# Kernel tuning notes

Hardware: AMD Instinct MI355X
Metric: run time of the kernel (lower is better)

## Reference

```python
import jax, jax.numpy as jnp
import numpy as np

B, S, D, d, O = 64, 196, 64, 2, 10  # batch, sites, bond_dim, feature dim, labels


def setup_inputs() -> dict:
    key = jax.random.key(0)
    k1, k2, k3 = jax.random.split(key, 3)
    x = jax.random.uniform(k1, (B, S, d), dtype=jnp.float32)
    # 'random_eye' init: identity on the bond indices (broadcast over input
    # index) plus small noise, so the untrained chain is well-conditioned.
    eye_cores = jnp.broadcast_to(jnp.eye(D, dtype=jnp.float32)[None, :, :, None], (S, D, D, d))
    cores = eye_cores + 0.01 * jax.random.normal(k2, (S, D, D, d), dtype=jnp.float32)
    out_core = 0.1 * jax.random.normal(k3, (O, D, D), dtype=jnp.float32)
    return {"x": x, "cores": cores, "out_core": out_core}


def _chain_matmul(mats):
    """Log-depth product of a chain of batched matrices. mats: [b, s, D, D]."""
    b, s, Dm, _ = mats.shape
    p = 1
    while p < s:
        p *= 2
    if p != s:  # pad with identities up to a power of two
        pad = jnp.broadcast_to(jnp.eye(Dm, dtype=mats.dtype), (b, p - s, Dm, Dm))
        mats = jnp.concatenate([mats, pad], axis=1)
    while mats.shape[1] > 1:  # pairwise tree reduction (log2(s) steps)
        mats = jnp.matmul(mats[:, 0::2], mats[:, 1::2])
    return mats[:, 0]  # [b, D, D]


def reference(x, cores, out_core):
    # InputRegion.forward: contract each site's feature vector with its core
    mats = jnp.einsum('slri,bsi->bslr', cores, x)  # [b, s, D, D]
    half = mats.shape[1] // 2  # output core sits at the chain center
    left = _chain_matmul(mats[:, :half])    # [b, D, D]
    right = _chain_matmul(mats[:, half:])   # [b, D, D]
    # Open boundary conditions: boundary vectors e0 = [1, 0, ..., 0]
    lvec = left[:, 0, :]   # e0 @ left  -> [b, D]
    rvec = right[:, :, 0]  # right @ e0 -> [b, D]
    # Contract through the central output core to get class scores
    return jnp.einsum('bl,olr,br->bo', lvec, out_core, rvec)  # [b, O]
```

## Files before the change

kernel.cpp:

```cpp
#include <hip/hip_runtime.h>

namespace {
constexpr int NB = 64, NS = 196, ND = 64, NO = 10;
constexpr int EPAIRS = NS * ND * ND;
constexpr size_t EBYTES = (size_t)EPAIRS * 4;


#define BARRIER() asm volatile("s_waitcnt lgkmcnt(0)\n\ts_barrier" ::: "memory")

#define U0(w_) __builtin_bit_cast(float, (unsigned)((w_) << 16))
#define U1(w_) __builtin_bit_cast(float, (unsigned)((w_) & 0xFFFF0000u))

__device__ __forceinline__ unsigned bf16rne(float f) {
    const unsigned b = __builtin_bit_cast(unsigned, f);
    return (b + 0x7FFFu + ((b >> 16) & 1u)) >> 16;
}

__global__ __launch_bounds__(256) void mps_conv_kernel(
    const float* __restrict__ cores, unsigned* __restrict__ etab)
{
    const int p = blockIdx.x * 256 + threadIdx.x;
    const int rem = p & 4095;
    const int l = rem >> 6, r = rem & 63;
    const float2 c = ((const float2*)cores)[p];
    const float sub = (l == r) ? 1.0f : 0.0f;
    etab[p] = bf16rne(c.x - sub) | (bf16rne(c.y - sub) << 16);
}

#define LLOAD(BUF, SITE) do {                                                 \
  const unsigned* _p = gL + (size_t)(SITE) * 4096;                            \
  _Pragma("unroll") for (int i = 0; i < 16; ++i)                              \
    BUF[i] = *(const uint2*)(_p + i * 64);                                    \
} while (0)

#define LSTEP(P, BUF, S) do {                                                 \
  const float2 xc = *(const float2*)(xlds + 2 * (S));                         \
  const float s0 = xc.x + xc.y;                                               \
  float4 vv[4];                                                               \
  _Pragma("unroll") for (int m = 0; m < 4; ++m)                               \
    vv[m] = ((const float4*)(vbuf[P] + 16 * q))[m];                           \
  const float2 yo = *(const float2*)(vbuf[P] + c0);                           \
  float a00a = 0.f, a10a = 0.f, a01a = 0.f, a11a = 0.f;                       \
  float a00b = 0.f, a10b = 0.f, a01b = 0.f, a11b = 0.f;                       \
  _Pragma("unroll") for (int i = 0; i < 16; i += 2) {                         \
    { const float vl = vv[i >> 2][i & 3]; const uint2 W = BUF[i];             \
      a00a = fmaf(vl, U0(W.x), a00a); a10a = fmaf(vl, U1(W.x), a10a);         \
      a01a = fmaf(vl, U0(W.y), a01a); a11a = fmaf(vl, U1(W.y), a11a); }       \
    { const float vl = vv[(i + 1) >> 2][(i + 1) & 3]; const uint2 W = BUF[i + 1]; \
      a00b = fmaf(vl, U0(W.x), a00b); a10b = fmaf(vl, U1(W.x), a10b);         \
      a01b = fmaf(vl, U0(W.y), a01b); a11b = fmaf(vl, U1(W.y), a11b); }       \
  }                                                                           \
  float a00 = a00a + a00b, a10 = a10a + a10b;                                 \
  float a01 = a01a + a01b, a11 = a11a + a11b;                                 \
  a00 += __shfl_xor(a00, 16, 64); a00 += __shfl_xor(a00, 32, 64);             \
  a10 += __shfl_xor(a10, 16, 64); a10 += __shfl_xor(a10, 32, 64);             \
  a01 += __shfl_xor(a01, 16, 64); a01 += __shfl_xor(a01, 32, 64);             \
  a11 += __shfl_xor(a11, 16, 64); a11 += __shfl_xor(a11, 32, 64);             \
  if (q == 0) {                                                               \
    float2 yn;                                                                \
    yn.x = fmaf(s0, yo.x, fmaf(xc.x, a00, xc.y * a10));                       \
    yn.y = fmaf(s0, yo.y, fmaf(xc.x, a01, xc.y * a11));                       \
    *(float2*)(vbuf[(P) ^ 1] + c0) = yn;                                      \
  }                                                                           \
} while (0)

#define RLOAD(BUF, SITE) do {                                                 \
  const unsigned* _p = gR + (size_t)(SITE) * 4096;                            \
  _Pragma("unroll") for (int m = 0; m < 8; ++m)                               \
    BUF[m] = *(const uint4*)(_p + m * 4);                                     \
} while (0)

#define RSTEP(P, BUF, K) do {                                                 \
  const float2 xc = *(const float2*)(xlds + 2 * (195 - (K)));                 \
  const float s0 = xc.x + xc.y;                                               \
  float4 vv[8];                                                               \
  _Pragma("unroll") for (int m = 0; m < 8; ++m)                               \
    vv[m] = ((const float4*)(vbuf[P] + 32 * h))[m];                           \
  const float yo = vbuf[P][row];                                              \
  float a0a = 0.f, a1a = 0.f, a0b = 0.f, a1b = 0.f;                           \
  _Pragma("unroll") for (int m = 0; m < 8; m += 2) {                          \
    { const uint4 W = BUF[m]; const float4 V = vv[m];                         \
      a0a = fmaf(V.x, U0(W.x), a0a); a1a = fmaf(V.x, U1(W.x), a1a);           \
      a0a = fmaf(V.y, U0(W.y), a0a); a1a = fmaf(V.y, U1(W.y), a1a);           \
      a0a = fmaf(V.z, U0(W.z), a0a); a1a = fmaf(V.z, U1(W.z), a1a);           \
      a0a = fmaf(V.w, U0(W.w), a0a); a1a = fmaf(V.w, U1(W.w), a1a); }         \
    { const uint4 W = BUF[m + 1]; const float4 V = vv[m + 1];                 \
      a0b = fmaf(V.x, U0(W.x), a0b); a1b = fmaf(V.x, U1(W.x), a1b);           \
      a0b = fmaf(V.y, U0(W.y), a0b); a1b = fmaf(V.y, U1(W.y), a1b);           \
      a0b = fmaf(V.z, U0(W.z), a0b); a1b = fmaf(V.z, U1(W.z), a1b);           \
      a0b = fmaf(V.w, U0(W.w), a0b); a1b = fmaf(V.w, U1(W.w), a1b); }         \
  }                                                                           \
  float a0 = a0a + a0b, a1 = a1a + a1b;                                       \
  a0 += __shfl_xor(a0, 1, 64);                                                \
  a1 += __shfl_xor(a1, 1, 64);                                                \
  if (h == 0)                                                                 \
    vbuf[(P) ^ 1][row] = fmaf(s0, yo, fmaf(xc.x, a0, xc.y * a1));             \
} while (0)

__global__ __launch_bounds__(128, 1) void mps_chain_kernel(
    const float* __restrict__ x,
    const unsigned* __restrict__ etab,
    float* __restrict__ wsv)
{
    __shared__ __align__(16) float vbuf[2][ND];
    __shared__ __align__(16) float xlds[NS * 2];

    const int bid   = blockIdx.x;
    const int batch = bid >> 1;
    const int dir   = bid & 1;
    const int tid   = threadIdx.x;
    const int w     = tid >> 6;
    const int lane  = tid & 63;

    for (int i = tid; i < 98; i += 128)
        ((float4*)xlds)[i] = ((const float4*)(x + batch * (NS * 2)))[i];
    if (tid < 64) vbuf[0][tid] = (tid == 0) ? 1.0f : 0.0f;
    __syncthreads();

    if (!dir) {
        const int q = lane >> 4, t = lane & 15;
        const int c0 = 32 * w + 2 * t;
        const unsigned* gL = etab + 16 * q * 64 + c0;
        uint2 eA[16], eB[16];
        LLOAD(eA, 0); LLOAD(eB, 1);
        #pragma unroll 1
        for (int s = 0; s < 96; s += 2) {
            LSTEP(0, eA, s);     LLOAD(eA, s + 2); BARRIER();
            LSTEP(1, eB, s + 1); LLOAD(eB, s + 3); BARRIER();
        }
        LSTEP(0, eA, 96); BARRIER();
        LSTEP(1, eB, 97); BARRIER();
    } else {
        const int lr = lane >> 1, h = lane & 1;
        const int row = 32 * w + lr;
        const unsigned* gR = etab + row * 64 + 32 * h;
        uint4 rA[8], rB[8];
        RLOAD(rA, 195); RLOAD(rB, 194);
        #pragma unroll 1
        for (int k = 0; k < 96; k += 2) {
            RSTEP(0, rA, k);     RLOAD(rA, 193 - k); BARRIER();
            RSTEP(1, rB, k + 1); RLOAD(rB, 192 - k); BARRIER();
        }
        RSTEP(0, rA, 96); BARRIER();
        RSTEP(1, rB, 97); BARRIER();
    }
    if (tid < 64) wsv[batch * 128 + dir * 64 + tid] = vbuf[0][tid];
}

__global__ __launch_bounds__(128) void mps_out_kernel(
    const float* __restrict__ wsv,
    const float* __restrict__ oc,
    float* __restrict__ out)
{
    __shared__ __align__(16) float lsh[ND];
    __shared__ __align__(16) float rsh[ND];
    const int b    = blockIdx.x;
    const int tid  = threadIdx.x;
    const int wave = tid >> 6;
    const int lane = tid & 63;
    if (wave == 0) lsh[lane] = wsv[b * 128 + lane];
    else           rsh[lane] = wsv[b * 128 + 64 + lane];
    __syncthreads();

    #pragma unroll
    for (int oo = 0; oo < 5; ++oo) {
        const int o = wave * 5 + oo;
        const float* ocp = oc + o * (ND * ND) + lane * ND;
        float acc = 0.f;
        #pragma unroll
        for (int t = 0; t < ND; t += 4) {
            const float4 r4 = *(const float4*)(rsh + t);
            const float4 c4 = *(const float4*)(ocp + t);
            acc = fmaf(c4.x, r4.x, acc);
            acc = fmaf(c4.y, r4.y, acc);
            acc = fmaf(c4.z, r4.z, acc);
            acc = fmaf(c4.w, r4.w, acc);
        }
        float p = lsh[lane] * acc;
        #pragma unroll
        for (int off = 32; off > 0; off >>= 1) p += __shfl_xor(p, off, 64);
        if (lane == 0) out[b * NO + o] = p;
    }
}
}

extern "C" void kernel_launch(void* const* d_in, const int* in_sizes, int n_in,
                              void* d_out, int out_size, void* d_ws, size_t ws_size,
                              hipStream_t stream) {
    const float* x     = (const float*)d_in[0];
    const float* cores = (const float*)d_in[1];
    const float* ocp   = (const float*)d_in[2];
    float* out = (float*)d_out;
    unsigned* etab = (unsigned*)d_ws;
    float* wsv = (float*)((char*)d_ws + EBYTES);
    hipLaunchKernelGGL(mps_conv_kernel,  dim3(EPAIRS / 256), dim3(256), 0, stream, cores, etab);
    hipLaunchKernelGGL(mps_chain_kernel, dim3(2 * NB), dim3(128), 0, stream, x, etab, wsv);
    hipLaunchKernelGGL(mps_out_kernel,   dim3(NB),     dim3(128), 0, stream, wsv, ocp, out);
}
```

Baseline: 69.54 us.

## Use inline-asm global loads with explicit vmcnt waits and register-held diagonal state

Replaces compiler-generated global loads of the bf16 core tables with inline-asm global_load instructions and places explicit s_waitcnt vmcnt(N) waits before each step. The aim is to keep the next site's prefetch in flight while the current site is computed, instead of letting the compiler insert a conservative full wait. It also keeps each thread's own vector element in a register rather than re-reading it from LDS, which removes one shared-memory load per step. Hand-managed wait counts are fragile: a wrong count, or the compiler reordering around the asm, could cause stale reads.

```diff
diff --git a/kernel.cpp b/kernel.cpp
--- a/kernel.cpp
+++ b/kernel.cpp
@@ -6,7 +6,14 @@
 constexpr size_t EBYTES = (size_t)EPAIRS * 4;
 
 
-#define BARRIER() asm volatile("s_waitcnt lgkmcnt(0)\n\ts_barrier" ::: "memory")
+#define SB0() __builtin_amdgcn_sched_barrier(0)
+#define WAITV(N) do { asm volatile("s_waitcnt vmcnt(" #N ")" ::: "memory"); SB0(); } while (0)
+#define BARRIER() do { asm volatile("s_waitcnt lgkmcnt(0)\n\ts_barrier" ::: "memory"); } while (0)
+
+#define GLX2(dst, ap, IMM) \
+  asm volatile("global_load_dwordx2 %0, %1, off offset:" #IMM : "=v"(dst) : "v"(ap))
+#define GLX4(dst, ap, IMM) \
+  asm volatile("global_load_dwordx4 %0, %1, off offset:" #IMM : "=v"(dst) : "v"(ap))
 
 #define U0(w_) __builtin_bit_cast(float, (unsigned)((w_) << 16))
 #define U1(w_) __builtin_bit_cast(float, (unsigned)((w_) & 0xFFFF0000u))
@@ -27,10 +34,24 @@
     etab[p] = bf16rne(c.x - sub) | (bf16rne(c.y - sub) << 16);
 }
 
-#define LLOAD(BUF, SITE) do {                                                 \
-  const unsigned* _p = gL + (size_t)(SITE) * 4096;                            \
-  _Pragma("unroll") for (int i = 0; i < 16; ++i)                              \
-    BUF[i] = *(const uint2*)(_p + i * 64);                                    \
+#define ALOADL(BUF, SITE) do {                                                \
+  const char* _a = gLb + (size_t)(SITE) * 16384;                              \
+  GLX2(BUF[0],  _a, 0);    GLX2(BUF[1],  _a, 256);                            \
+  GLX2(BUF[2],  _a, 512);  GLX2(BUF[3],  _a, 768);                            \
+  GLX2(BUF[4],  _a, 1024); GLX2(BUF[5],  _a, 1280);                           \
+  GLX2(BUF[6],  _a, 1536); GLX2(BUF[7],  _a, 1792);                           \
+  GLX2(BUF[8],  _a, 2048); GLX2(BUF[9],  _a, 2304);                           \
+  GLX2(BUF[10], _a, 2560); GLX2(BUF[11], _a, 2816);                           \
+  GLX2(BUF[12], _a, 3072); GLX2(BUF[13], _a, 3328);                           \
+  GLX2(BUF[14], _a, 3584); GLX2(BUF[15], _a, 3840);                           \
+} while (0)
+
+#define ALOADR(BUF, SITE) do {                                                \
+  const char* _a = gRb + (size_t)(SITE) * 16384;                              \
+  GLX4(BUF[0], _a, 0);  GLX4(BUF[1], _a, 16);                                 \
+  GLX4(BUF[2], _a, 32); GLX4(BUF[3], _a, 48);                                 \
+  GLX4(BUF[4], _a, 64); GLX4(BUF[5], _a, 80);                                 \
+  GLX4(BUF[6], _a, 96); GLX4(BUF[7], _a, 112);                                \
 } while (0)
 
 #define LSTEP(P, BUF, S) do {                                                 \
@@ -39,7 +60,6 @@
   float4 vv[4];                                                               \
   _Pragma("unroll") for (int m = 0; m < 4; ++m)                               \
     vv[m] = ((const float4*)(vbuf[P] + 16 * q))[m];                           \
-  const float2 yo = *(const float2*)(vbuf[P] + c0);                           \
   float a00a = 0.f, a10a = 0.f, a01a = 0.f, a11a = 0.f;                       \
   float a00b = 0.f, a10b = 0.f, a01b = 0.f, a11b = 0.f;                       \
   _Pragma("unroll") for (int i = 0; i < 16; i += 2) {                         \
@@ -56,18 +76,12 @@
   a10 += __shfl_xor(a10, 16, 64); a10 += __shfl_xor(a10, 32, 64);             \
   a01 += __shfl_xor(a01, 16, 64); a01 += __shfl_xor(a01, 32, 64);             \
   a11 += __shfl_xor(a11, 16, 64); a11 += __shfl_xor(a11, 32, 64);             \
+  y0r = fmaf(s0, y0r, fmaf(xc.x, a00, xc.y * a10));                           \
+  y1r = fmaf(s0, y1r, fmaf(xc.x, a01, xc.y * a11));                           \
   if (q == 0) {                                                               \
-    float2 yn;                                                                \
-    yn.x = fmaf(s0, yo.x, fmaf(xc.x, a00, xc.y * a10));                       \
-    yn.y = fmaf(s0, yo.y, fmaf(xc.x, a01, xc.y * a11));                       \
+    float2 yn; yn.x = y0r; yn.y = y1r;                                        \
     *(float2*)(vbuf[(P) ^ 1] + c0) = yn;                                      \
   }                                                                           \
-} while (0)
-
-#define RLOAD(BUF, SITE) do {                                                 \
-  const unsigned* _p = gR + (size_t)(SITE) * 4096;                            \
-  _Pragma("unroll") for (int m = 0; m < 8; ++m)                               \
-    BUF[m] = *(const uint4*)(_p + m * 4);                                     \
 } while (0)
 
 #define RSTEP(P, BUF, K) do {                                                 \
@@ -76,7 +90,6 @@
   float4 vv[8];                                                               \
   _Pragma("unroll") for (int m = 0; m < 8; ++m)                               \
     vv[m] = ((const float4*)(vbuf[P] + 32 * h))[m];                           \
-  const float yo = vbuf[P][row];                                              \
   float a0a = 0.f, a1a = 0.f, a0b = 0.f, a1b = 0.f;                           \
   _Pragma("unroll") for (int m = 0; m < 8; m += 2) {                          \
     { const uint4 W = BUF[m]; const float4 V = vv[m];                         \
@@ -93,8 +106,8 @@
   float a0 = a0a + a0b, a1 = a1a + a1b;                                       \
   a0 += __shfl_xor(a0, 1, 64);                                                \
   a1 += __shfl_xor(a1, 1, 64);                                                \
-  if (h == 0)                                                                 \
-    vbuf[(P) ^ 1][row] = fmaf(s0, yo, fmaf(xc.x, a0, xc.y * a1));             \
+  yr = fmaf(s0, yr, fmaf(xc.x, a0, xc.y * a1));                               \
+  if (h == 0) vbuf[(P) ^ 1][row] = yr;                                        \
 } while (0)
 
 __global__ __launch_bounds__(128, 1) void mps_chain_kernel(
@@ -120,29 +133,31 @@
     if (!dir) {
         const int q = lane >> 4, t = lane & 15;
         const int c0 = 32 * w + 2 * t;
-        const unsigned* gL = etab + 16 * q * 64 + c0;
+        const char* gLb = (const char*)(etab + 16 * q * 64 + c0);
+        float y0r = (c0 == 0) ? 1.f : 0.f, y1r = 0.f;
         uint2 eA[16], eB[16];
-        LLOAD(eA, 0); LLOAD(eB, 1);
+        ALOADL(eA, 0); ALOADL(eB, 1);
         #pragma unroll 1
         for (int s = 0; s < 96; s += 2) {
-            LSTEP(0, eA, s);     LLOAD(eA, s + 2); BARRIER();
-            LSTEP(1, eB, s + 1); LLOAD(eB, s + 3); BARRIER();
+            WAITV(16); LSTEP(0, eA, s);     ALOADL(eA, s + 2); BARRIER();
+            WAITV(16); LSTEP(1, eB, s + 1); ALOADL(eB, s + 3); BARRIER();
         }
-        LSTEP(0, eA, 96); BARRIER();
-        LSTEP(1, eB, 97); BARRIER();
+        WAITV(16); LSTEP(0, eA, 96); BARRIER();
+        WAITV(0);  LSTEP(1, eB, 97); BARRIER();
     } else {
         const int lr = lane >> 1, h = lane & 1;
         const int row = 32 * w + lr;
-        const unsigned* gR = etab + row * 64 + 32 * h;
+        const char* gRb = (const char*)(etab + row * 64 + 32 * h);
+        float yr = (row == 0) ? 1.f : 0.f;
         uint4 rA[8], rB[8];
-        RLOAD(rA, 195); RLOAD(rB, 194);
+        ALOADR(rA, 195); ALOADR(rB, 194);
         #pragma unroll 1
         for (int k = 0; k < 96; k += 2) {
-            RSTEP(0, rA, k);     RLOAD(rA, 193 - k); BARRIER();
-            RSTEP(1, rB, k + 1); RLOAD(rB, 192 - k); BARRIER();
+            WAITV(8); RSTEP(0, rA, k);     ALOADR(rA, 193 - k); BARRIER();
+            WAITV(8); RSTEP(1, rB, k + 1); ALOADR(rB, 192 - k); BARRIER();
         }
-        RSTEP(0, rA, 96); BARRIER();
-        RSTEP(1, rB, 97); BARRIER();
+        WAITV(8); RSTEP(0, rA, 96); BARRIER();
+        WAITV(0); RSTEP(1, rB, 97); BARRIER();
     }
     if (tid < 64) wsv[batch * 128 + dir * 64 + tid] = vbuf[0][tid];
 }
```

Result: faster. 66.36 us (-4.6%).
